# Kernel tuning notes

Measured on AMD Instinct MI355X. Metric: run time of the kernel, lower is better.

## Reference

```python
import jax, jax.numpy as jnp
import numpy as np

D_MODEL, D_FF, N_EXPERTS, TOP_K = 768, 3072, 8, 2
B, S = 2, 1024
LN_EPS = 1e-5


def setup_inputs() -> dict:
    key = jax.random.key(0)
    k1, k2, k3, k4 = jax.random.split(key, 4)
    return {
        "hidden_states": jax.random.normal(k1, (B, S, D_MODEL), dtype=jnp.float32),
        "ln_gamma": jnp.ones((D_MODEL,), dtype=jnp.float32),
        "ln_beta": jnp.zeros((D_MODEL,), dtype=jnp.float32),
        "router_w": jax.random.normal(k2, (D_MODEL, N_EXPERTS), dtype=jnp.float32) * 0.02,
        "w1": jax.random.normal(k3, (N_EXPERTS, D_MODEL, D_FF), dtype=jnp.float32) * 0.02,
        "w2": jax.random.normal(k4, (N_EXPERTS, D_FF, D_MODEL), dtype=jnp.float32) * 0.02,
    }


def _layernorm(x, gamma, beta):
    mu = jnp.mean(x, axis=-1, keepdims=True)
    var = jnp.mean(jnp.square(x - mu), axis=-1, keepdims=True)
    return (x - mu) * jax.lax.rsqrt(var + LN_EPS) * gamma + beta


def reference(hidden_states, ln_gamma, ln_beta, router_w, w1, w2):
    Bz, Sz, D = hidden_states.shape
    residual = hidden_states
    x = _layernorm(hidden_states, ln_gamma, ln_beta)
    tokens = x.reshape(-1, D)                       # [T, D]
    T = tokens.shape[0]

    # Router: softmax over experts, top-k selection, gate normalization
    logits = tokens @ router_w                      # [T, E]
    probs = jax.nn.softmax(logits, axis=-1)
    topw, topi = jax.lax.top_k(probs, TOP_K)        # [T, K]
    topw = topw / jnp.sum(topw, axis=-1, keepdims=True)  # normalize_gates=True

    # Dense gate matrix [T, E] (zero for unselected experts)
    gates = jnp.zeros((T, N_EXPERTS), dtype=tokens.dtype)
    gates = gates.at[jnp.arange(T)[:, None], topi].set(topw)

    # Per-expert FFN (silu, no bias), weighted combine
    h = jnp.einsum('td,edf->etf', tokens, w1)       # [E, T, F]
    h = jax.nn.silu(h)
    y = jnp.einsum('etf,efd->etd', h, w2)           # [E, T, D]
    out = jnp.einsum('te,etd->td', gates, y)        # [T, D]

    return residual + out.reshape(Bz, Sz, D)
```

## Files before the change

### kernel.cpp

```cpp
#include <hip/hip_runtime.h>
#include <hip/hip_bf16.h>
#include <math.h>

#define T_TOK 2048
#define DM 768
#define DF 3072
#define NE 8

typedef __attribute__((ext_vector_type(4))) float f32x4;
typedef __attribute__((ext_vector_type(8))) short bf16x8;
typedef __attribute__((ext_vector_type(8))) unsigned short u16x8;

static __device__ __forceinline__ ushort f2bf(float f) {
    union { float f; unsigned u; } x; x.f = f;
    unsigned r = x.u + 0x7fff + ((x.u >> 16) & 1);
    return (ushort)(r >> 16);
}
static __device__ __forceinline__ float bf2f(ushort u) {
    union { unsigned u; float f; } x; x.u = ((unsigned)u) << 16; return x.f;
}

__global__ __launch_bounds__(256) void ln_router_kernel(
    const float* __restrict__ hs, const float* __restrict__ gamma,
    const float* __restrict__ beta, const float* __restrict__ rw,
    ushort* __restrict__ xbf, float* __restrict__ topw, int* __restrict__ topi,
    int* __restrict__ counts)
{
    int t = blockIdx.x;
    int tid = threadIdx.x;
    const float* row = hs + (size_t)t * DM;
    float v[3];
    v[0] = row[tid]; v[1] = row[tid + 256]; v[2] = row[tid + 512];
    float s  = v[0] + v[1] + v[2];
    float sq = v[0]*v[0] + v[1]*v[1] + v[2]*v[2];
    #pragma unroll
    for (int off = 32; off > 0; off >>= 1) {
        s  += __shfl_down(s, off);
        sq += __shfl_down(sq, off);
    }
    __shared__ float wsum[4], wsq[4];
    __shared__ float pl[4][8];
    int lane = tid & 63, wv = tid >> 6;
    if (lane == 0) { wsum[wv] = s; wsq[wv] = sq; }
    __syncthreads();
    float tot  = wsum[0] + wsum[1] + wsum[2] + wsum[3];
    float totq = wsq[0] + wsq[1] + wsq[2] + wsq[3];
    float mu = tot * (1.0f / 768.0f);
    float var = totq * (1.0f / 768.0f) - mu * mu;
    float rstd = rsqrtf(var + 1e-5f);

    float p[8];
    #pragma unroll
    for (int e = 0; e < 8; e++) p[e] = 0.f;
    #pragma unroll
    for (int i = 0; i < 3; i++) {
        int d = tid + i * 256;
        float yv = (v[i] - mu) * rstd * gamma[d] + beta[d];
        xbf[(size_t)t * DM + d] = f2bf(yv);
        const float* r8 = rw + (size_t)d * 8;
        #pragma unroll
        for (int e = 0; e < 8; e++) p[e] += yv * r8[e];
    }
    #pragma unroll
    for (int off = 32; off > 0; off >>= 1) {
        #pragma unroll
        for (int e = 0; e < 8; e++) p[e] += __shfl_down(p[e], off);
    }
    if (lane == 0) {
        #pragma unroll
        for (int e = 0; e < 8; e++) pl[wv][e] = p[e];
    }
    __syncthreads();
    if (tid == 0) {
        float lg[8];
        #pragma unroll
        for (int e = 0; e < 8; e++) lg[e] = pl[0][e] + pl[1][e] + pl[2][e] + pl[3][e];
        int i0 = 0; float l0 = lg[0];
        #pragma unroll
        for (int e = 1; e < 8; e++) if (lg[e] > l0) { l0 = lg[e]; i0 = e; }
        int i1 = -1; float l1 = -3.4e38f;
        #pragma unroll
        for (int e = 0; e < 8; e++) if (e != i0 && lg[e] > l1) { l1 = lg[e]; i1 = e; }
        float w0 = 1.0f / (1.0f + __expf(l1 - l0));
        topi[2 * t] = i0;  topi[2 * t + 1] = i1;
        topw[2 * t] = w0;  topw[2 * t + 1] = 1.0f - w0;
        atomicAdd(&counts[i0], 1);
        atomicAdd(&counts[i1], 1);
    }
}

__global__ void scan_kernel(int* __restrict__ ctl)
{
    if (threadIdx.x == 0 && blockIdx.x == 0) {
        int acc = 0;
        for (int e = 0; e < 8; e++) {
            ctl[8 + e] = acc;
            acc += ctl[e];
            ctl[16 + e] = 0;
        }
    }
}

__global__ __launch_bounds__(256) void bucket_kernel(
    const int* __restrict__ topi, int* __restrict__ ctl,
    int* __restrict__ bucket_tok, int* __restrict__ tok_slot)
{
    int t = blockIdx.x * 256 + threadIdx.x;
    if (t >= T_TOK) return;
    #pragma unroll
    for (int k = 0; k < 2; k++) {
        int e = topi[2 * t + k];
        int pos = atomicAdd(&ctl[16 + e], 1);
        int idx = ctl[8 + e] + pos;
        bucket_tok[idx] = t;
        tok_slot[2 * t + k] = idx;
    }
}

__global__ __launch_bounds__(256) void wconv_kernel(
    const float* __restrict__ w1, const float* __restrict__ w2,
    ushort* __restrict__ w1t, ushort* __restrict__ w2t)
{
    int mat = blockIdx.y;
    int e = mat & 7;
    bool isw2 = mat >= 8;
    int R = isw2 ? DF : DM;
    int Cc = isw2 ? DM : DF;
    const float* src = (isw2 ? w2 : w1) + (size_t)e * R * Cc;
    ushort* dst = (isw2 ? w2t : w1t) + (size_t)e * R * Cc;
    int tiles_c = Cc >> 6;
    int tc = blockIdx.x % tiles_c;
    int tr = blockIdx.x / tiles_c;
    int c0 = tc << 6, r0 = tr << 6;
    __shared__ float tile[64][65];
    int tx = threadIdx.x & 15, ty = threadIdx.x >> 4;
    #pragma unroll
    for (int j = 0; j < 4; j++) {
        int r = ty + j * 16;
        float4 v = *(const float4*)&src[(size_t)(r0 + r) * Cc + c0 + tx * 4];
        tile[r][tx*4+0] = v.x; tile[r][tx*4+1] = v.y;
        tile[r][tx*4+2] = v.z; tile[r][tx*4+3] = v.w;
    }
    __syncthreads();
    int n  = threadIdx.x >> 2;
    int kc = (threadIdx.x & 3) * 16;
    u16x8 a, b;
    #pragma unroll
    for (int q = 0; q < 8; q++) {
        a[q] = f2bf(tile[kc + q][n]);
        b[q] = f2bf(tile[kc + 8 + q][n]);
    }
    ushort* dp = &dst[(size_t)(c0 + n) * R + r0 + kc];
    *(u16x8*)dp = a;
    *(u16x8*)(dp + 8) = b;
}

template<bool SILU, bool GATHER, int NT, int SPLITS>
__global__ __launch_bounds__(256) void moe_gemm(
    const ushort* __restrict__ A, const ushort* __restrict__ Bt,
    ushort* __restrict__ C, const int* __restrict__ ctl,
    const int* __restrict__ bucket_tok, int K, int N)
{
    int bid = blockIdx.x;
    int e = bid & 7;
    int j = bid >> 3;
    int mt = j & 15;
    int c = j >> 4;
    int nt = c % NT;
    int sk = c / NT;
    int cnt = ctl[e];
    if (mt * 128 >= cnt) return;
    int off = ctl[8 + e];
    const int Ks = K / SPLITS;
    int kbase = sk * Ks;

    __shared__ ushort Al[2][128 * 32];
    __shared__ ushort Bl[2][128 * 32];

    int tid = threadIdx.x, lane = tid & 63, wv = tid >> 6;
    int kchunk = (lane & 3) * 8;

    const ushort* aptr[2];
    #pragma unroll
    for (int i = 0; i < 2; i++) {
        int r = i * 64 + wv * 16 + (lane >> 2);
        int gr = mt * 128 + r;
        if (gr >= cnt) gr = cnt - 1;
        if (GATHER) aptr[i] = A + (size_t)bucket_tok[off + gr] * K;
        else        aptr[i] = A + (size_t)(off + gr) * K;
    }
    const ushort* bptr[2];
    size_t bbase = (size_t)e * N * K;
    #pragma unroll
    for (int i = 0; i < 2; i++) {
        int n = nt * 128 + i * 64 + wv * 16 + (lane >> 2);
        bptr[i] = Bt + bbase + (size_t)n * K;
    }

    f32x4 acc[4][4];
    #pragma unroll
    for (int m = 0; m < 4; m++)
        #pragma unroll
        for (int n = 0; n < 4; n++)
            acc[m][n] = (f32x4){0.f, 0.f, 0.f, 0.f};

    int wr = wv >> 1, wc = wv & 1;
    int l15 = lane & 15, kq = lane >> 4;
    int ldst = (wv * 16) * 32 + lane * 8;

    auto stage = [&](int buf, int k0) {
        #pragma unroll
        for (int i = 0; i < 2; i++) {
            __builtin_amdgcn_global_load_lds(
                (const __attribute__((address_space(1))) void*)(aptr[i] + k0 + kchunk),
                (__attribute__((address_space(3))) void*)(&Al[buf][i * 64 * 32 + ldst]),
                16, 0, 0);
            __builtin_amdgcn_global_load_lds(
                (const __attribute__((address_space(1))) void*)(bptr[i] + k0 + kchunk),
                (__attribute__((address_space(3))) void*)(&Bl[buf][i * 64 * 32 + ldst]),
                16, 0, 0);
        }
    };

    const int nk = Ks >> 5;
    stage(0, kbase);
    asm volatile("s_waitcnt vmcnt(0)" ::: "memory");
    __builtin_amdgcn_s_barrier();

    for (int ks = 0; ks < nk; ks++) {
        int cur = ks & 1;
        if (ks + 1 < nk) stage(cur ^ 1, kbase + (ks + 1) * 32);
        bf16x8 af[4], bfr[4];
        #pragma unroll
        for (int m = 0; m < 4; m++)
            af[m] = *(const bf16x8*)&Al[cur][(wr * 64 + m * 16 + l15) * 32 + kq * 8];
        #pragma unroll
        for (int n = 0; n < 4; n++)
            bfr[n] = *(const bf16x8*)&Bl[cur][(wc * 64 + n * 16 + l15) * 32 + kq * 8];
        __builtin_amdgcn_s_setprio(1);
        #pragma unroll
        for (int m = 0; m < 4; m++)
            #pragma unroll
            for (int n = 0; n < 4; n++)
                acc[m][n] = __builtin_amdgcn_mfma_f32_16x16x32_bf16(af[m], bfr[n], acc[m][n], 0, 0, 0);
        __builtin_amdgcn_s_setprio(0);
        asm volatile("s_waitcnt vmcnt(0) lgkmcnt(0)" ::: "memory");
        __builtin_amdgcn_s_barrier();
    }

    #pragma unroll
    for (int m = 0; m < 4; m++) {
        #pragma unroll
        for (int n = 0; n < 4; n++) {
            #pragma unroll
            for (int jj = 0; jj < 4; jj++) {
                int gr = mt * 128 + wr * 64 + m * 16 + kq * 4 + jj;
                if (gr < cnt) {
                    float v = acc[m][n][jj];
                    if (SILU) v = v / (1.0f + __expf(-v));
                    int col = nt * 128 + wc * 64 + n * 16 + l15;
                    C[((size_t)sk * (T_TOK * 2) + off + gr) * N + col] = f2bf(v);
                }
            }
        }
    }
}

template<int SPLITS>
__global__ __launch_bounds__(256) void combine_kernel(
    const float* __restrict__ hs, const ushort* __restrict__ Yp,
    const float* __restrict__ topw, const int* __restrict__ tok_slot,
    float* __restrict__ out)
{
    int t = blockIdx.x, tid = threadIdx.x;
    int s0 = tok_slot[2 * t], s1 = tok_slot[2 * t + 1];
    float w0 = topw[2 * t], w1 = topw[2 * t + 1];
    const float* h = hs + (size_t)t * DM;
    float* o = out + (size_t)t * DM;
    #pragma unroll
    for (int i = 0; i < 3; i++) {
        int d = tid + i * 256;
        float y0 = 0.f, y1 = 0.f;
        #pragma unroll
        for (int s = 0; s < SPLITS; s++) {
            y0 += bf2f(Yp[((size_t)s * (T_TOK * 2) + s0) * DM + d]);
            y1 += bf2f(Yp[((size_t)s * (T_TOK * 2) + s1) * DM + d]);
        }
        o[d] = h[d] + w0 * y0 + w1 * y1;
    }
}

extern "C" void kernel_launch(void* const* d_in, const int* in_sizes, int n_in,
                              void* d_out, int out_size, void* d_ws, size_t ws_size,
                              hipStream_t stream)
{
    const float* hs    = (const float*)d_in[0];
    const float* gamma = (const float*)d_in[1];
    const float* beta  = (const float*)d_in[2];
    const float* rw    = (const float*)d_in[3];
    const float* w1    = (const float*)d_in[4];
    const float* w2    = (const float*)d_in[5];
    float* out = (float*)d_out;
    char* ws = (char*)d_ws;

    size_t o = 0;
    auto alc = [&](size_t b) { size_t r = o; o += (b + 255) & ~255ULL; return r; };
    int*    ctl        = (int*)(ws + alc(256));
    float*  topw       = (float*)(ws + alc((size_t)T_TOK * 2 * 4));
    int*    topi       = (int*)(ws + alc((size_t)T_TOK * 2 * 4));
    int*    tok_slot   = (int*)(ws + alc((size_t)T_TOK * 2 * 4));
    int*    bucket_tok = (int*)(ws + alc((size_t)T_TOK * 2 * 4));
    ushort* xbf        = (ushort*)(ws + alc((size_t)T_TOK * DM * 2));
    ushort* w1t        = (ushort*)(ws + alc((size_t)NE * DF * DM * 2));
    ushort* w2t        = (ushort*)(ws + alc((size_t)NE * DF * DM * 2));
    ushort* Hg         = (ushort*)(ws + alc((size_t)T_TOK * 2 * DF * 2));
    size_t yp_off      = alc((size_t)4 * T_TOK * 2 * DM * 2);
    ushort* Yp         = (ushort*)(ws + yp_off);
    bool can_split     = (o <= ws_size);

    hipMemsetAsync(ctl, 0, 256, stream);
    wconv_kernel<<<dim3(576, 16), 256, 0, stream>>>(w1, w2, w1t, w2t);
    ln_router_kernel<<<T_TOK, 256, 0, stream>>>(hs, gamma, beta, rw, xbf, topw, topi, ctl);
    scan_kernel<<<1, 64, 0, stream>>>(ctl);
    bucket_kernel<<<8, 256, 0, stream>>>(topi, ctl, bucket_tok, tok_slot);

    moe_gemm<true, true, 24, 1><<<8 * 16 * 24, 256, 0, stream>>>(
        xbf, w1t, Hg, ctl, bucket_tok, DM, DF);

    if (can_split) {
        moe_gemm<false, false, 6, 4><<<8 * 16 * 6 * 4, 256, 0, stream>>>(
            Hg, w2t, Yp, ctl, bucket_tok, DF, DM);
        combine_kernel<4><<<T_TOK, 256, 0, stream>>>(hs, Yp, topw, tok_slot, out);
    } else {
        moe_gemm<false, false, 6, 1><<<8 * 16 * 6, 256, 0, stream>>>(
            Hg, w2t, Yp, ctl, bucket_tok, DF, DM);
        combine_kernel<1><<<T_TOK, 256, 0, stream>>>(hs, Yp, topw, tok_slot, out);
    }
}
```

Baseline: 222.8 us.

## Pack weights as K-pair bf16 without transpose and drop scan kernel

Replaces the LDS-tiled transpose conversion of the fp32 weights with a streaming pack kernel. It stores pairs of consecutive K rows as packed bf16 words in the original row-major N layout, so the conversion becomes a coalesced elementwise pass. The GEMM's B tile loading and LDS fragment reads are rewritten for this layout, using an XOR swizzle to avoid bank conflicts at the cost of four scalar LDS reads per fragment instead of one vector read. The separate scan kernel is removed, and expert offsets are recomputed inline from the counts in the bucket and GEMM kernels, saving one launch.

Measured after the change: 220.3 us. About the same (-1.1%).

```diff
diff --git a/kernel.cpp b/kernel.cpp
--- a/kernel.cpp
+++ b/kernel.cpp
@@ -9,7 +9,6 @@
 
 typedef __attribute__((ext_vector_type(4))) float f32x4;
 typedef __attribute__((ext_vector_type(8))) short bf16x8;
-typedef __attribute__((ext_vector_type(8))) unsigned short u16x8;
 
 static __device__ __forceinline__ ushort f2bf(float f) {
     union { float f; unsigned u; } x; x.f = f;
@@ -18,6 +17,9 @@
 }
 static __device__ __forceinline__ float bf2f(ushort u) {
     union { unsigned u; float f; } x; x.u = ((unsigned)u) << 16; return x.f;
+}
+static __device__ __forceinline__ unsigned pk2(float lo, float hi) {
+    return (unsigned)f2bf(lo) | ((unsigned)f2bf(hi) << 16);
 }
 
 __global__ __launch_bounds__(256) void ln_router_kernel(
@@ -89,75 +91,49 @@
     }
 }
 
-__global__ void scan_kernel(int* __restrict__ ctl)
-{
-    if (threadIdx.x == 0 && blockIdx.x == 0) {
-        int acc = 0;
-        for (int e = 0; e < 8; e++) {
-            ctl[8 + e] = acc;
-            acc += ctl[e];
-            ctl[16 + e] = 0;
-        }
-    }
-}
-
 __global__ __launch_bounds__(256) void bucket_kernel(
     const int* __restrict__ topi, int* __restrict__ ctl,
     int* __restrict__ bucket_tok, int* __restrict__ tok_slot)
 {
     int t = blockIdx.x * 256 + threadIdx.x;
     if (t >= T_TOK) return;
+    int offs[8]; int acc = 0;
+    #pragma unroll
+    for (int e = 0; e < 8; e++) { offs[e] = acc; acc += ctl[e]; }
     #pragma unroll
     for (int k = 0; k < 2; k++) {
         int e = topi[2 * t + k];
         int pos = atomicAdd(&ctl[16 + e], 1);
-        int idx = ctl[8 + e] + pos;
+        int idx = offs[e] + pos;
         bucket_tok[idx] = t;
         tok_slot[2 * t + k] = idx;
     }
 }
 
-__global__ __launch_bounds__(256) void wconv_kernel(
+__global__ __launch_bounds__(256) void wpack_kernel(
     const float* __restrict__ w1, const float* __restrict__ w2,
-    ushort* __restrict__ w1t, ushort* __restrict__ w2t)
-{
-    int mat = blockIdx.y;
-    int e = mat & 7;
-    bool isw2 = mat >= 8;
-    int R = isw2 ? DF : DM;
-    int Cc = isw2 ? DM : DF;
-    const float* src = (isw2 ? w2 : w1) + (size_t)e * R * Cc;
-    ushort* dst = (isw2 ? w2t : w1t) + (size_t)e * R * Cc;
-    int tiles_c = Cc >> 6;
-    int tc = blockIdx.x % tiles_c;
-    int tr = blockIdx.x / tiles_c;
-    int c0 = tc << 6, r0 = tr << 6;
-    __shared__ float tile[64][65];
-    int tx = threadIdx.x & 15, ty = threadIdx.x >> 4;
-    #pragma unroll
-    for (int j = 0; j < 4; j++) {
-        int r = ty + j * 16;
-        float4 v = *(const float4*)&src[(size_t)(r0 + r) * Cc + c0 + tx * 4];
-        tile[r][tx*4+0] = v.x; tile[r][tx*4+1] = v.y;
-        tile[r][tx*4+2] = v.z; tile[r][tx*4+3] = v.w;
-    }
-    __syncthreads();
-    int n  = threadIdx.x >> 2;
-    int kc = (threadIdx.x & 3) * 16;
-    u16x8 a, b;
-    #pragma unroll
-    for (int q = 0; q < 8; q++) {
-        a[q] = f2bf(tile[kc + q][n]);
-        b[q] = f2bf(tile[kc + 8 + q][n]);
-    }
-    ushort* dp = &dst[(size_t)(c0 + n) * R + r0 + kc];
-    *(u16x8*)dp = a;
-    *(u16x8*)(dp + 8) = b;
+    unsigned* __restrict__ w1p, unsigned* __restrict__ w2p)
+{
+    const size_t MQ = (size_t)NE * DM * DF / 8;
+    size_t stride = (size_t)gridDim.x * 256;
+    for (size_t i = (size_t)blockIdx.x * 256 + threadIdx.x; i < 2 * MQ; i += stride) {
+        bool m2 = i >= MQ;
+        size_t o = (m2 ? i - MQ : i) * 4;
+        int N = m2 ? DM : DF;
+        size_t n = o % (size_t)N;
+        const float* src = (m2 ? w2 : w1) + 2 * o - n;
+        float4 a = *(const float4*)src;
+        float4 b = *(const float4*)(src + N);
+        uint4 r;
+        r.x = pk2(a.x, b.x); r.y = pk2(a.y, b.y);
+        r.z = pk2(a.z, b.z); r.w = pk2(a.w, b.w);
+        *(uint4*)((m2 ? w2p : w1p) + o) = r;
+    }
 }
 
 template<bool SILU, bool GATHER, int NT, int SPLITS>
 __global__ __launch_bounds__(256) void moe_gemm(
-    const ushort* __restrict__ A, const ushort* __restrict__ Bt,
+    const ushort* __restrict__ A, const unsigned* __restrict__ Bp,
     ushort* __restrict__ C, const int* __restrict__ ctl,
     const int* __restrict__ bucket_tok, int K, int N)
 {
@@ -170,12 +146,14 @@
     int sk = c / NT;
     int cnt = ctl[e];
     if (mt * 128 >= cnt) return;
-    int off = ctl[8 + e];
+    int off = 0;
+    #pragma unroll
+    for (int q = 0; q < 8; q++) if (q < e) off += ctl[q];
     const int Ks = K / SPLITS;
     int kbase = sk * Ks;
 
     __shared__ ushort Al[2][128 * 32];
-    __shared__ ushort Bl[2][128 * 32];
+    __shared__ unsigned Bl[2][16 * 128];
 
     int tid = threadIdx.x, lane = tid & 63, wv = tid >> 6;
     int kchunk = (lane & 3) * 8;
@@ -189,12 +167,16 @@
         if (GATHER) aptr[i] = A + (size_t)bucket_tok[off + gr] * K;
         else        aptr[i] = A + (size_t)(off + gr) * K;
     }
-    const ushort* bptr[2];
-    size_t bbase = (size_t)e * N * K;
-    #pragma unroll
-    for (int i = 0; i < 2; i++) {
-        int n = nt * 128 + i * 64 + wv * 16 + (lane >> 2);
-        bptr[i] = Bt + bbase + (size_t)n * K;
+    const unsigned* Bb = Bp + (size_t)e * ((size_t)N * (K / 2));
+    int n0 = nt * 128;
+    int brow2[2], bscol[2];
+    #pragma unroll
+    for (int ii = 0; ii < 2; ii++) {
+        int g = wv * 2 + ii;
+        int row2 = 2 * g + (lane >> 5);
+        int col4 = 4 * (lane & 31);
+        brow2[ii] = row2;
+        bscol[ii] = col4 ^ ((row2 & 7) << 2);
     }
 
     f32x4 acc[4][4];
@@ -206,18 +188,24 @@
 
     int wr = wv >> 1, wc = wv & 1;
     int l15 = lane & 15, kq = lane >> 4;
-    int ldst = (wv * 16) * 32 + lane * 8;
+    int ldstA = (wv * 16) * 32 + lane * 8;
+    int xk = (kq & 1) << 4;
 
     auto stage = [&](int buf, int k0) {
         #pragma unroll
         for (int i = 0; i < 2; i++) {
             __builtin_amdgcn_global_load_lds(
                 (const __attribute__((address_space(1))) void*)(aptr[i] + k0 + kchunk),
-                (__attribute__((address_space(3))) void*)(&Al[buf][i * 64 * 32 + ldst]),
+                (__attribute__((address_space(3))) void*)(&Al[buf][i * 64 * 32 + ldstA]),
                 16, 0, 0);
+        }
+        int k2b = k0 >> 1;
+        #pragma unroll
+        for (int ii = 0; ii < 2; ii++) {
+            int g = wv * 2 + ii;
             __builtin_amdgcn_global_load_lds(
-                (const __attribute__((address_space(1))) void*)(bptr[i] + k0 + kchunk),
-                (__attribute__((address_space(3))) void*)(&Bl[buf][i * 64 * 32 + ldst]),
+                (const __attribute__((address_space(1))) void*)(Bb + (size_t)(k2b + brow2[ii]) * N + n0 + bscol[ii]),
+                (__attribute__((address_space(3))) void*)(&Bl[buf][g * 256 + lane * 4]),
                 16, 0, 0);
         }
     };
@@ -234,9 +222,17 @@
         #pragma unroll
         for (int m = 0; m < 4; m++)
             af[m] = *(const bf16x8*)&Al[cur][(wr * 64 + m * 16 + l15) * 32 + kq * 8];
-        #pragma unroll
-        for (int n = 0; n < 4; n++)
-            bfr[n] = *(const bf16x8*)&Bl[cur][(wc * 64 + n * 16 + l15) * 32 + kq * 8];
+        const unsigned* Blc = &Bl[cur][0];
+        #pragma unroll
+        for (int n = 0; n < 4; n++) {
+            int ncol = wc * 64 + n * 16 + l15;
+            union { uint4 u; bf16x8 h; } cvu;
+            cvu.u.x = Blc[(kq * 4 + 0) * 128 + (ncol ^ (xk | 0))];
+            cvu.u.y = Blc[(kq * 4 + 1) * 128 + (ncol ^ (xk | 4))];
+            cvu.u.z = Blc[(kq * 4 + 2) * 128 + (ncol ^ (xk | 8))];
+            cvu.u.w = Blc[(kq * 4 + 3) * 128 + (ncol ^ (xk | 12))];
+            bfr[n] = cvu.h;
+        }
         __builtin_amdgcn_s_setprio(1);
         #pragma unroll
         for (int m = 0; m < 4; m++)
@@ -305,35 +301,34 @@
 
     size_t o = 0;
     auto alc = [&](size_t b) { size_t r = o; o += (b + 255) & ~255ULL; return r; };
-    int*    ctl        = (int*)(ws + alc(256));
-    float*  topw       = (float*)(ws + alc((size_t)T_TOK * 2 * 4));
-    int*    topi       = (int*)(ws + alc((size_t)T_TOK * 2 * 4));
-    int*    tok_slot   = (int*)(ws + alc((size_t)T_TOK * 2 * 4));
-    int*    bucket_tok = (int*)(ws + alc((size_t)T_TOK * 2 * 4));
-    ushort* xbf        = (ushort*)(ws + alc((size_t)T_TOK * DM * 2));
-    ushort* w1t        = (ushort*)(ws + alc((size_t)NE * DF * DM * 2));
-    ushort* w2t        = (ushort*)(ws + alc((size_t)NE * DF * DM * 2));
-    ushort* Hg         = (ushort*)(ws + alc((size_t)T_TOK * 2 * DF * 2));
-    size_t yp_off      = alc((size_t)4 * T_TOK * 2 * DM * 2);
-    ushort* Yp         = (ushort*)(ws + yp_off);
-    bool can_split     = (o <= ws_size);
+    int*      ctl        = (int*)(ws + alc(256));
+    float*    topw       = (float*)(ws + alc((size_t)T_TOK * 2 * 4));
+    int*      topi       = (int*)(ws + alc((size_t)T_TOK * 2 * 4));
+    int*      tok_slot   = (int*)(ws + alc((size_t)T_TOK * 2 * 4));
+    int*      bucket_tok = (int*)(ws + alc((size_t)T_TOK * 2 * 4));
+    ushort*   xbf        = (ushort*)(ws + alc((size_t)T_TOK * DM * 2));
+    unsigned* w1p        = (unsigned*)(ws + alc((size_t)NE * DF * DM * 2));
+    unsigned* w2p        = (unsigned*)(ws + alc((size_t)NE * DF * DM * 2));
+    ushort*   Hg         = (ushort*)(ws + alc((size_t)T_TOK * 2 * DF * 2));
+    size_t yp_off        = alc((size_t)4 * T_TOK * 2 * DM * 2);
+    ushort*   Yp         = (ushort*)(ws + yp_off);
+    bool can_split       = (o <= ws_size);
 
     hipMemsetAsync(ctl, 0, 256, stream);
-    wconv_kernel<<<dim3(576, 16), 256, 0, stream>>>(w1, w2, w1t, w2t);
+    wpack_kernel<<<2048, 256, 0, stream>>>(w1, w2, w1p, w2p);
     ln_router_kernel<<<T_TOK, 256, 0, stream>>>(hs, gamma, beta, rw, xbf, topw, topi, ctl);
-    scan_kernel<<<1, 64, 0, stream>>>(ctl);
     bucket_kernel<<<8, 256, 0, stream>>>(topi, ctl, bucket_tok, tok_slot);
 
     moe_gemm<true, true, 24, 1><<<8 * 16 * 24, 256, 0, stream>>>(
-        xbf, w1t, Hg, ctl, bucket_tok, DM, DF);
+        xbf, w1p, Hg, ctl, bucket_tok, DM, DF);
 
     if (can_split) {
         moe_gemm<false, false, 6, 4><<<8 * 16 * 6 * 4, 256, 0, stream>>>(
-            Hg, w2t, Yp, ctl, bucket_tok, DF, DM);
+            Hg, w2p, Yp, ctl, bucket_tok, DF, DM);
         combine_kernel<4><<<T_TOK, 256, 0, stream>>>(hs, Yp, topw, tok_slot, out);
     } else {
         moe_gemm<false, false, 6, 1><<<8 * 16 * 6, 256, 0, stream>>>(
-            Hg, w2t, Yp, ctl, bucket_tok, DF, DM);
+            Hg, w2p, Yp, ctl, bucket_tok, DF, DM);
         combine_kernel<1><<<T_TOK, 256, 0, stream>>>(hs, Yp, topw, tok_slot, out);
     }
 }
```
